# Kernel optimization log

Measured on AMD Instinct MI355X. Metric: run time of the kernel, lower is better.

## Reference

```python
import jax, jax.numpy as jnp
import numpy as np

# dims
T, B, N, H = 16, 8, 8, 128            # time, batch, num_schemas, schema_dim
C, IH, IW = 32, 16, 16                # conv_dims
TASK, ACT, REW = 128, 16, 1
HEADS = 7
TAR = TASK + ACT + REW                # 145
CTX = H + TAR                         # 273 context_dim
CONV_FLAT = C * IH * IW               # 8192
MEM_IN = CONV_FLAT + H + CTX          # 8593


def setup_inputs() -> dict:
    key = jax.random.key(0)
    ks = jax.random.split(key, 20)
    def n(k, shape, s=0.02):
        return jax.random.normal(k, shape, dtype=jnp.float32) * s
    D = HEADS * H
    return {
        "image": jax.random.normal(ks[0], (T, B, C, IH, IW), dtype=jnp.float32),
        "task_action_reward": jax.random.normal(ks[1], (T, B, TAR), dtype=jnp.float32),
        # MultiHeadedAttention params
        "Wq_w": n(ks[2], (D, CTX)), "Wq_b": jnp.zeros((D,), jnp.float32),
        "Wk_w": n(ks[3], (D, H)),   "Wk_b": jnp.zeros((D,), jnp.float32),
        "Wv_w": n(ks[4], (D, H)),   "Wv_b": jnp.zeros((D,), jnp.float32),
        "Wo_w": n(ks[5], (H, D)),   "Wo_b": jnp.zeros((H,), jnp.float32),
        # TopdownFeatureAttention: N per-query linears (stacked) + 1x1 conv
        "td_w": n(ks[6], (N, C, CTX)), "td_b": jnp.zeros((N, C), jnp.float32),
        "conv_w": n(ks[7], (C, C)), "conv_b": jnp.zeros((C,), jnp.float32),
        # ListStructuredRnn: N per-schema LSTM cells (PyTorch gate order i,f,g,o)
        "Wih": n(ks[8], (N, 4 * H, MEM_IN)), "Whh": n(ks[9], (N, 4 * H, H)),
        "bih": jnp.zeros((N, 4 * H), jnp.float32), "bhh": jnp.zeros((N, 4 * H), jnp.float32),
    }


def reference(image, task_action_reward, Wq_w, Wq_b, Wk_w, Wk_b, Wv_w, Wv_b,
              Wo_w, Wo_b, td_w, td_b, conv_w, conv_b, Wih, Whh, bih, bhh):
    f32 = image.dtype
    # prev_state=None path: prev_h is zeros for all timesteps
    prev_h = jnp.zeros((T, B, N, H), f32)
    # schema_context = duplicate task_action_reward over schemas, cat prev_h -> (T,B,N,CTX)
    ctx = jnp.concatenate(
        [jnp.broadcast_to(task_action_reward[:, :, None, :], (T, B, N, TAR)), prev_h], axis=-1)
    # keys = cat(prev_h, zeros) along schema axis -> (T,B,N+1,H)
    keys = jnp.concatenate([prev_h, jnp.zeros((T, B, 1, H), f32)], axis=2)

    # --- MultiHeadedAttention (no mask; dropout unused in forward) ---
    q = (ctx @ Wq_w.T + Wq_b).reshape(T, B, N, HEADS, H)
    k = (keys @ Wk_w.T + Wk_b).reshape(T, B, N + 1, HEADS, H)
    v = (keys @ Wv_w.T + Wv_b).reshape(T, B, N + 1, HEADS, H)
    scores = jnp.einsum('tbqhd,tbkhd->tbhqk', q, k) / jnp.sqrt(jnp.asarray(H, f32))
    attn = jax.nn.softmax(scores, axis=-1)
    xatt = jnp.einsum('tbhqk,tbkhd->tbqhd', attn, v).reshape(T, B, N, HEADS * H)
    shared = xatt @ Wo_w.T + Wo_b                      # (T,B,N,H)

    # --- TopdownFeatureAttention: per-query linear -> sigmoid channel gate -> 1x1 conv ---
    gate = jax.nn.sigmoid(jnp.einsum('tbnx,ncx->tbnc', ctx, td_w) + td_b)   # (T,B,N,C)
    modulated = image[:, :, None] * gate[..., None, None]                    # (T,B,N,C,IH,IW)
    conv = jnp.einsum('tbnchw,dc->tbndhw', modulated, conv_w) + conv_b[:, None, None]
    schema_updates = conv.reshape(T, B, N, CONV_FLAT)

    # --- per-schema LSTMs over time (zero initial state) ---
    mem = jnp.concatenate([schema_updates, shared, ctx], axis=-1)            # (T,B,N,MEM_IN)
    xg = jnp.einsum('tbni,ngi->tbng', mem, Wih) + bih + bhh                  # (T,B,N,4H)

    def step(carry, g_t):
        h, c = carry
        g = g_t + jnp.einsum('bnh,ngh->bng', h, Whh)
        i, f, gg, o = jnp.split(g, 4, axis=-1)
        c = jax.nn.sigmoid(f) * c + jax.nn.sigmoid(i) * jnp.tanh(gg)
        h = jax.nn.sigmoid(o) * jnp.tanh(c)
        return (h, c), h

    z = jnp.zeros((B, N, H), f32)
    (hT, cT), hs = jax.lax.scan(step, (z, z), xg)
    outs = hs.reshape(T, B, N * H)
    return outs, hT, cT
```

## Files before the change

kernel.cpp:

```cpp
#include <hip/hip_runtime.h>

#define T_   16
#define B_   8
#define N_   8
#define H_   128
#define C_   32
#define HW_  256
#define TAR_ 145
#define G4H  512
#define MEMIN 8593
#define AK   8512
#define XGN  524288
#define KSTEP 64
#define PANEL_E 136192

typedef __attribute__((ext_vector_type(8))) short short8v;
typedef __attribute__((ext_vector_type(4))) float f32x4;
typedef __attribute__((ext_vector_type(4), aligned(4))) float f32x4u;

__device__ __forceinline__ float bf2f(unsigned short u){
  return __uint_as_float(((unsigned int)u) << 16);
}
__device__ __forceinline__ unsigned short f2bf(float x){
  unsigned int b = __float_as_uint(x);
  return (unsigned short)((b + 0x7fffu + ((b >> 16) & 1u)) >> 16);
}
__device__ __forceinline__ unsigned pkbf(float lo, float hi){
  return __builtin_amdgcn_perm(__float_as_uint(hi) + 0x8000u,
                               __float_as_uint(lo) + 0x8000u, 0x07060302u);
}
__device__ __forceinline__ float bflo(unsigned w){ return __uint_as_float(w << 16); }
__device__ __forceinline__ float bfhi(unsigned w){ return __uint_as_float(w & 0xffff0000u); }
__device__ __forceinline__ float sigf(float x){ return 1.f/(1.f + expf(-x)); }

__device__ __forceinline__ void gl_lds16(const void* g, void* l){
  __builtin_amdgcn_global_load_lds(
      (const __attribute__((address_space(1))) unsigned int*)g,
      (__attribute__((address_space(3))) unsigned int*)l, 16, 0, 0);
}
__device__ __forceinline__ void gl_lds4(const void* g, void* l){
  __builtin_amdgcn_global_load_lds(
      (const __attribute__((address_space(1))) unsigned int*)g,
      (__attribute__((address_space(3))) unsigned int*)l, 4, 0, 0);
}

__global__ void k_shared(const float* __restrict__ WvB, const float* __restrict__ WoW,
                         const float* __restrict__ WoB, float* __restrict__ sh){
  const int h = blockIdx.x, lane = threadIdx.x;
  float acc = 0.f;
  for(int d = lane; d < 896; d += 64) acc += WvB[d] * WoW[h*896 + d];
  for(int s = 32; s; s >>= 1) acc += __shfl_down(acc, s);
  if(lane == 0) sh[h] = acc + WoB[h];
}

__global__ __launch_bounds__(256) void k_gate(const float* __restrict__ tar,
                                              const float* __restrict__ tdw,
                                              const float* __restrict__ tdb,
                                              float* __restrict__ gate){
  __shared__ float twS[32*145];
  __shared__ float taS[16*145];
  const int tb0 = blockIdx.x * 16, n = blockIdx.y, tid = threadIdx.x;
  for(int i = tid; i < 32*145; i += 256){
    int c = i / 145, x = i - c*145;
    twS[i] = tdw[(n*32 + c)*273 + x];
  }
  for(int i = tid; i < 16*145; i += 256)
    taS[i] = tar[tb0*145 + i];
  __syncthreads();
  for(int o = tid; o < 512; o += 256){
    int r = o >> 5, c = o & 31;
    float a = tdb[n*32 + c];
    const float* tr = &taS[r*145];
    const float* tw = &twS[c*145];
    for(int x = 0; x < 145; ++x) a += tr[x]*tw[x];
    gate[((tb0 + r)*N_ + n)*C_ + c] = 1.f/(1.f + expf(-a));
  }
}

__global__ __launch_bounds__(256) void k_conv2(
    const float* __restrict__ img, const float* __restrict__ gate,
    const float* __restrict__ cw, const float* __restrict__ cb,
    const float* __restrict__ sh, const float* __restrict__ tar,
    unsigned short* __restrict__ mem)
{
  __shared__ float imgS[8192];
  __shared__ float cwgT[1024];
  const int tb = blockIdx.x, n = blockIdx.y;
  const int hw = threadIdx.x;
  for(int i = hw; i < 8192; i += 256)
    imgS[i] = img[(size_t)tb*8192 + i];
  for(int i = hw; i < 1024; i += 256){
    const int c = i >> 5, d = i & 31;
    cwgT[i] = cw[d*32 + c] * gate[(tb*8 + n)*32 + c];
  }
  __syncthreads();
  f32x4 acc[8];
  #pragma unroll
  for(int dq = 0; dq < 8; ++dq){
    const f32x4u cv = *(const f32x4u*)&cb[dq*4];
    acc[dq].x = cv.x; acc[dq].y = cv.y; acc[dq].z = cv.z; acc[dq].w = cv.w;
  }
  #pragma unroll 4
  for(int c = 0; c < 32; ++c){
    const float iv = imgS[c*256 + hw];
    #pragma unroll
    for(int dq = 0; dq < 8; ++dq){
      const f32x4 w = *(const f32x4*)&cwgT[c*32 + dq*4];
      acc[dq].x += iv*w.x; acc[dq].y += iv*w.y;
      acc[dq].z += iv*w.z; acc[dq].w += iv*w.w;
    }
  }
  unsigned short* mrow = mem + (size_t)(n*128 + tb)*AK;
  #pragma unroll
  for(int dq = 0; dq < 8; ++dq){
    mrow[(dq*4 + 0)*256 + hw] = f2bf(acc[dq].x);
    mrow[(dq*4 + 1)*256 + hw] = f2bf(acc[dq].y);
    mrow[(dq*4 + 2)*256 + hw] = f2bf(acc[dq].z);
    mrow[(dq*4 + 3)*256 + hw] = f2bf(acc[dq].w);
  }
  for(int i = hw; i < 320; i += 256){
    if(i < 128)      mrow[8192 + i]       = f2bf(sh[i]);
    else if(i < 273) mrow[8320 + i - 128] = f2bf(tar[tb*TAR_ + i - 128]);
    else             mrow[8465 + i - 273] = 0;
  }
}

__global__ __launch_bounds__(256) void k_wprep(
    const float* __restrict__ Wih, unsigned short* __restrict__ wsB)
{
  const unsigned J = 4358144u;
  const unsigned stride = gridDim.x * 256u;
  for(unsigned j = blockIdx.x*256u + threadIdx.x; j < J; j += stride){
    const unsigned r  = j / 1064u;
    const unsigned k0 = (j - r*1064u) * 8u;
    const float* src = Wih + (size_t)r*MEMIN + k0;
    const f32x4u v0 = *(const f32x4u*)src;
    const f32x4u v1 = *(const f32x4u*)(src + 4);
    uint4 o;
    o.x = pkbf(v0.x, v0.y); o.y = pkbf(v0.z, v0.w);
    o.z = pkbf(v1.x, v1.y); o.w = pkbf(v1.z, v1.w);
    const unsigned n = r >> 9, g512 = r & 511u;
    const unsigned gt = g512 >> 4, g = g512 & 15u;
    const unsigned kb = k0 >> 6, kin = k0 & 63u;
    const unsigned ksw = (((kin >> 3) ^ (g & 7u)) << 3);
    unsigned short* dst = wsB + (size_t)(n*32u + gt)*PANEL_E
                          + kb*1024u + g*64u + ksw;
    *(uint4*)dst = o;
  }
}

__global__ __launch_bounds__(256) void k_gemm6(
    const unsigned short* __restrict__ mem, const unsigned short* __restrict__ wsB,
    float* __restrict__ xg4)
{
  __shared__ unsigned short Abuf[2][128*64];
  __shared__ unsigned short Bbuf[2][16*64];
  const int gt = blockIdx.x, n = blockIdx.y, ks = blockIdx.z;
  const int tid = threadIdx.x;
  const int wv = tid >> 6, ln = tid & 63;
  const int lr = ln & 15, lg = ln >> 4;
  const int g0 = gt*16;
  const int kbeg = (ks == 0) ? 0 : 2176 + (ks - 1)*2112;
  const int nsteps = (ks == 0) ? 34 : 33;
  const unsigned short* An = mem + (size_t)n*128*AK;
  const char* panelB = (const char*)(wsB + (size_t)(n*32 + gt)*PANEL_E);

#define STAGE6(bb, kk) do{                                                     \
    _Pragma("unroll")                                                          \
    for(int i_ = 0; i_ < 4; ++i_){                                             \
      const int ci_ = i_*256 + tid;                                            \
      const int row_ = ci_ >> 3;                                               \
      const unsigned short* src_ = An + (size_t)row_*AK + (kk)                 \
                                   + (((ci_ & 7) ^ (row_ & 7)) << 3);          \
      gl_lds16(src_, &Abuf[bb][(i_*256 + wv*64)*8]);                           \
    }                                                                          \
    _Pragma("unroll")                                                          \
    for(int j_ = 0; j_ < 2; ++j_){                                             \
      const char* srcB_ = panelB + (size_t)((kk) >> 6)*2048                    \
                          + wv*512 + j_*256 + ln*4;                            \
      gl_lds4(srcB_, (char*)&Bbuf[bb][0] + wv*512 + j_*256);                   \
    }                                                                          \
  }while(0)

  f32x4 acc0 = {0.f,0.f,0.f,0.f};
  f32x4 acc1 = {0.f,0.f,0.f,0.f};

  STAGE6(0, kbeg);
  __syncthreads();

  int b = 0;
  for(int t = 0; t < nsteps; ++t){
    if(t + 1 < nsteps) STAGE6(b^1, kbeg + (t+1)*KSTEP);
    #pragma unroll
    for(int s = 0; s < 2; ++s){
      const int jb = (s*4 + lg) ^ (lr & 7);
      const short8v bf = *(const short8v*)&Bbuf[b][lr*64 + jb*8];
      const short8v a0 = *(const short8v*)&Abuf[b][(wv*32 + lr)*64 + jb*8];
      const short8v a1 = *(const short8v*)&Abuf[b][(wv*32 + 16 + lr)*64 + jb*8];
      acc0 = __builtin_amdgcn_mfma_f32_16x16x32_bf16(a0, bf, acc0, 0, 0, 0);
      acc1 = __builtin_amdgcn_mfma_f32_16x16x32_bf16(a1, bf, acc1, 0, 0, 0);
    }
    __syncthreads();
    b ^= 1;
  }
#undef STAGE6

  float* dst = xg4 + (size_t)ks*XGN;
  const int c0 = g0 + lr;
  const int r0 = wv*32 + lg*4, r1 = r0 + 16;
  #pragma unroll
  for(int j = 0; j < 4; ++j){
    dst[(size_t)((r0 + j)*8 + n)*G4H + c0] = acc0[j];
    dst[(size_t)((r1 + j)*8 + n)*G4H + c0] = acc1[j];
  }
}

__global__ __launch_bounds__(256) void k_gemm5(
    const unsigned short* __restrict__ mem, const float* __restrict__ Wih,
    float* __restrict__ xg4)
{
  __shared__ unsigned short Abuf[2][128*64];
  __shared__ float          Bbuf[2][16*64];
  const int gt = blockIdx.x, n = blockIdx.y, ks = blockIdx.z;
  const int tid = threadIdx.x;
  const int wv = tid >> 6, ln = tid & 63;
  const int lr = ln & 15, lg = ln >> 4;
  const int g0 = gt*16;
  const int kbeg = (ks == 0) ? 0 : 2176 + (ks - 1)*2112;
  const int nsteps = (ks == 0) ? 34 : 33;
  const unsigned short* An = mem + (size_t)n*128*AK;
  const float* Bn = Wih + (size_t)(n*G4H + g0)*MEMIN;

#define STAGE5(bb, kk) do{                                                     \
    _Pragma("unroll")                                                          \
    for(int i_ = 0; i_ < 4; ++i_){                                             \
      const int ci_ = i_*256 + tid;                                            \
      const int row_ = ci_ >> 3;                                               \
      const unsigned short* src_ = An + (size_t)row_*AK + (kk)                 \
                                   + (((ci_ & 7) ^ (row_ & 7)) << 3);          \
      gl_lds16(src_, &Abuf[bb][(i_*256 + wv*64)*8]);                           \
    }                                                                          \
    _Pragma("unroll")                                                          \
    for(int q_ = 0; q_ < 4; ++q_){                                             \
      const int idx_ = q_*256 + tid;                                           \
      const int g_ = idx_ >> 6;                                                \
      const int kd_ = idx_ & 63;                                               \
      const float* srcB_ = Bn + (size_t)g_*MEMIN + (kk)                        \
                           + ((((kd_ >> 3) ^ (g_ & 7)) << 3) + (kd_ & 7));     \
      gl_lds4(srcB_, &Bbuf[bb][q_*256 + wv*64]);                               \
    }                                                                          \
  }while(0)

  f32x4 acc0 = {0.f,0.f,0.f,0.f};
  f32x4 acc1 = {0.f,0.f,0.f,0.f};

  STAGE5(0, kbeg);
  if(nsteps > 1) STAGE5(1, kbeg + KSTEP);

  int b = 0;
  for(int t = 0; t < nsteps; ++t){
    if(t < nsteps - 1){
      asm volatile("s_waitcnt vmcnt(8)" ::: "memory");
    } else {
      asm volatile("s_waitcnt vmcnt(0)" ::: "memory");
    }
    __builtin_amdgcn_s_barrier();
    #pragma unroll
    for(int s = 0; s < 2; ++s){
      const int jb = (s*4 + lg) ^ (lr & 7);
      const float* bp = &Bbuf[b][lr*64 + jb*8];
      const f32x4 blo = *(const f32x4*)bp;
      const f32x4 bhi = *(const f32x4*)(bp + 4);
      short8v bf;
      unsigned* u = (unsigned*)&bf;
      u[0] = pkbf(blo.x, blo.y); u[1] = pkbf(blo.z, blo.w);
      u[2] = pkbf(bhi.x, bhi.y); u[3] = pkbf(bhi.z, bhi.w);
      const short8v a0 = *(const short8v*)&Abuf[b][(wv*32 + lr)*64 + jb*8];
      const short8v a1 = *(const short8v*)&Abuf[b][(wv*32 + 16 + lr)*64 + jb*8];
      acc0 = __builtin_amdgcn_mfma_f32_16x16x32_bf16(a0, bf, acc0, 0, 0, 0);
      acc1 = __builtin_amdgcn_mfma_f32_16x16x32_bf16(a1, bf, acc1, 0, 0, 0);
    }
    __builtin_amdgcn_s_barrier();
    if(t + 2 < nsteps) STAGE5(b, kbeg + (t+2)*KSTEP);
    b ^= 1;
  }
#undef STAGE5

  float* dst = xg4 + (size_t)ks*XGN;
  const int c0 = g0 + lr;
  const int r0 = wv*32 + lg*4, r1 = r0 + 16;
  #pragma unroll
  for(int j = 0; j < 4; ++j){
    dst[(size_t)((r0 + j)*8 + n)*G4H + c0] = acc0[j];
    dst[(size_t)((r1 + j)*8 + n)*G4H + c0] = acc1[j];
  }
}

__global__ __launch_bounds__(512) void k_lstm2(
    const float* __restrict__ xg4, const float* __restrict__ Whh,
    const float* __restrict__ bih, const float* __restrict__ bhh,
    float* __restrict__ out)
{
  __shared__ float hS[128];
  __shared__ float preS[512];
  const int bn = blockIdx.x;
  const int n = bn & 7, b = bn >> 3;
  const int g = threadIdx.x;

  unsigned wr[64];
  const float* wrow = Whh + (size_t)(n*G4H + g)*H_;
  #pragma unroll
  for(int i = 0; i < 32; ++i){
    const f32x4 w = *(const f32x4*)(wrow + i*4);
    wr[2*i]   = pkbf(w.x, w.y);
    wr[2*i+1] = pkbf(w.z, w.w);
  }
  const float bias = bih[n*G4H + g] + bhh[n*G4H + g];
  if(g < 128) hS[g] = 0.f;
  float cc = 0.f;
  __syncthreads();

  for(int t = 0; t < 16; ++t){
    const size_t xb = (size_t)((t*8 + b)*8 + n)*G4H + g;
    float acc = bias + xg4[xb] + xg4[xb + XGN] + xg4[xb + 2*XGN] + xg4[xb + 3*XGN];
    #pragma unroll
    for(int q = 0; q < 32; ++q){
      const f32x4 hv = *(const f32x4*)&hS[q*4];
      const unsigned w0 = wr[2*q], w1 = wr[2*q+1];
      acc += hv.x*bflo(w0) + hv.y*bfhi(w0) + hv.z*bflo(w1) + hv.w*bfhi(w1);
    }
    preS[g] = acc;
    __syncthreads();
    if(g < 128){
      const float iv = sigf(preS[g]);
      const float fv = sigf(preS[128 + g]);
      const float gv = tanhf(preS[256 + g]);
      const float ov = sigf(preS[384 + g]);
      cc = fv*cc + iv*gv;
      const float hn = ov*tanhf(cc);
      hS[g] = hn;
      out[(t*8 + b)*1024 + n*128 + g] = hn;
      if(t == 15){
        out[131072 + (b*8 + n)*128 + g] = hn;
        out[139264 + (b*8 + n)*128 + g] = cc;
      }
    }
    __syncthreads();
  }
}

extern "C" void kernel_launch(void* const* d_in, const int* in_sizes, int n_in,
                              void* d_out, int out_size, void* d_ws, size_t ws_size,
                              hipStream_t stream)
{
  (void)in_sizes; (void)n_in; (void)out_size;
  const float* img  = (const float*)d_in[0];
  const float* tar  = (const float*)d_in[1];
  const float* WvB  = (const float*)d_in[7];
  const float* WoW  = (const float*)d_in[8];
  const float* WoB  = (const float*)d_in[9];
  const float* tdw  = (const float*)d_in[10];
  const float* tdb  = (const float*)d_in[11];
  const float* cw   = (const float*)d_in[12];
  const float* cb   = (const float*)d_in[13];
  const float* Wih  = (const float*)d_in[14];
  const float* Whh  = (const float*)d_in[15];
  const float* bih  = (const float*)d_in[16];
  const float* bhh  = (const float*)d_in[17];

  float* wsf   = (float*)d_ws;
  float* gatew = wsf;
  float* shw   = wsf + 32768;
  float* xg4w  = wsf + 32896;
  unsigned short* memA = (unsigned short*)((char*)d_ws + 8520192);
  unsigned short* wsB  = (unsigned short*)((char*)d_ws + 25952768);
  const size_t WS_A  = 25952768;
  const size_t WS_AP = 25952768 + (size_t)256*PANEL_E*2;

  k_shared<<<128, 64, 0, stream>>>(WvB, WoW, WoB, shw);
  k_gate<<<dim3(8, 8), 256, 0, stream>>>(tar, tdw, tdb, gatew);
  k_conv2<<<dim3(128, 8), 256, 0, stream>>>(img, gatew, cw, cb, shw, tar, memA);

  if(ws_size >= WS_AP){
    k_wprep<<<2048, 256, 0, stream>>>(Wih, wsB);
    k_gemm6<<<dim3(32, 8, 4), 256, 0, stream>>>(memA, wsB, xg4w);
  } else if(ws_size >= WS_A){
    k_gemm5<<<dim3(32, 8, 4), 256, 0, stream>>>(memA, Wih, xg4w);
  }
  k_lstm2<<<64, 512, 0, stream>>>(xg4w, Whh, bih, bhh, (float*)d_out);
}
```

Before: 146.9 us.

## Replace weight-prep plus split-K GEMM with single fp32-B 4-stage pipelined GEMM

Removes the separate bf16 weight-packing kernel and the 4-way split-K of the input-projection GEMM. A new kernel streams fp32 Wih straight into LDS through a 4-slot ring buffer with explicit vmcnt waits, converts it to bf16 at fragment load, and runs the full K range in one block per (schema, gate tile), 256 blocks. The LSTM kernel now takes the number of partial sums as a parameter, so it reads one partial instead of four. The cost is twice the B bytes staged in LDS, more dynamic shared memory per block, and less parallelism than the 1024-block split-K grid.

```diff
diff --git a/kernel.cpp b/kernel.cpp
--- a/kernel.cpp
+++ b/kernel.cpp
@@ -12,7 +12,6 @@
 #define AK   8512
 #define XGN  524288
 #define KSTEP 64
-#define PANEL_E 136192
 
 typedef __attribute__((ext_vector_type(8))) short short8v;
 typedef __attribute__((ext_vector_type(4))) float f32x4;
@@ -125,93 +124,138 @@
   }
 }
 
-__global__ __launch_bounds__(256) void k_wprep(
-    const float* __restrict__ Wih, unsigned short* __restrict__ wsB)
-{
-  const unsigned J = 4358144u;
-  const unsigned stride = gridDim.x * 256u;
-  for(unsigned j = blockIdx.x*256u + threadIdx.x; j < J; j += stride){
-    const unsigned r  = j / 1064u;
-    const unsigned k0 = (j - r*1064u) * 8u;
-    const float* src = Wih + (size_t)r*MEMIN + k0;
-    const f32x4u v0 = *(const f32x4u*)src;
-    const f32x4u v1 = *(const f32x4u*)(src + 4);
-    uint4 o;
-    o.x = pkbf(v0.x, v0.y); o.y = pkbf(v0.z, v0.w);
-    o.z = pkbf(v1.x, v1.y); o.w = pkbf(v1.z, v1.w);
-    const unsigned n = r >> 9, g512 = r & 511u;
-    const unsigned gt = g512 >> 4, g = g512 & 15u;
-    const unsigned kb = k0 >> 6, kin = k0 & 63u;
-    const unsigned ksw = (((kin >> 3) ^ (g & 7u)) << 3);
-    unsigned short* dst = wsB + (size_t)(n*32u + gt)*PANEL_E
-                          + kb*1024u + g*64u + ksw;
-    *(uint4*)dst = o;
-  }
-}
-
-__global__ __launch_bounds__(256) void k_gemm6(
-    const unsigned short* __restrict__ mem, const unsigned short* __restrict__ wsB,
-    float* __restrict__ xg4)
-{
-  __shared__ unsigned short Abuf[2][128*64];
-  __shared__ unsigned short Bbuf[2][16*64];
-  const int gt = blockIdx.x, n = blockIdx.y, ks = blockIdx.z;
+__global__ __launch_bounds__(256) void k_gemm7(
+    const unsigned short* __restrict__ mem, const float* __restrict__ Wih,
+    float* __restrict__ xg)
+{
+  extern __shared__ char smem7[];
+  unsigned short (*Abuf)[128*64] = (unsigned short(*)[128*64])smem7;
+  float (*Bbuf)[16*64] = (float(*)[16*64])(smem7 + 4*128*64*2);
+  const int bid = blockIdx.x;
+  const int n = bid & 7, gt = bid >> 3;
   const int tid = threadIdx.x;
   const int wv = tid >> 6, ln = tid & 63;
   const int lr = ln & 15, lg = ln >> 4;
   const int g0 = gt*16;
-  const int kbeg = (ks == 0) ? 0 : 2176 + (ks - 1)*2112;
-  const int nsteps = (ks == 0) ? 34 : 33;
   const unsigned short* An = mem + (size_t)n*128*AK;
-  const char* panelB = (const char*)(wsB + (size_t)(n*32 + gt)*PANEL_E);
-
-#define STAGE6(bb, kk) do{                                                     \
+  const float* Bn = Wih + (size_t)(n*G4H + g0)*MEMIN;
+
+#define STAGE7(sl, kk) do{                                                     \
     _Pragma("unroll")                                                          \
     for(int i_ = 0; i_ < 4; ++i_){                                             \
       const int ci_ = i_*256 + tid;                                            \
       const int row_ = ci_ >> 3;                                               \
       const unsigned short* src_ = An + (size_t)row_*AK + (kk)                 \
                                    + (((ci_ & 7) ^ (row_ & 7)) << 3);          \
-      gl_lds16(src_, &Abuf[bb][(i_*256 + wv*64)*8]);                           \
+      gl_lds16(src_, &Abuf[sl][(i_*256 + wv*64)*8]);                           \
     }                                                                          \
     _Pragma("unroll")                                                          \
-    for(int j_ = 0; j_ < 2; ++j_){                                             \
-      const char* srcB_ = panelB + (size_t)((kk) >> 6)*2048                    \
-                          + wv*512 + j_*256 + ln*4;                            \
-      gl_lds4(srcB_, (char*)&Bbuf[bb][0] + wv*512 + j_*256);                   \
+    for(int q_ = 0; q_ < 4; ++q_){                                             \
+      const int idx_ = q_*256 + tid;                                           \
+      const int g_ = idx_ >> 6;                                                \
+      const int kd_ = idx_ & 63;                                               \
+      const float* srcB_ = Bn + (size_t)g_*MEMIN + (kk)                        \
+                           + ((((kd_ >> 3) ^ (g_ & 7)) << 3) + (kd_ & 7));     \
+      gl_lds4(srcB_, &Bbuf[sl][q_*256 + wv*64]);                               \
     }                                                                          \
   }while(0)
 
   f32x4 acc0 = {0.f,0.f,0.f,0.f};
   f32x4 acc1 = {0.f,0.f,0.f,0.f};
 
-  STAGE6(0, kbeg);
-  __syncthreads();
-
-  int b = 0;
-  for(int t = 0; t < nsteps; ++t){
-    if(t + 1 < nsteps) STAGE6(b^1, kbeg + (t+1)*KSTEP);
+  STAGE7(0, 0);
+  STAGE7(1, KSTEP);
+  STAGE7(2, 2*KSTEP);
+
+  for(int t = 0; t < 133; ++t){
+    if(t < 131){
+      asm volatile("s_waitcnt vmcnt(16)" ::: "memory");
+    } else if(t == 131){
+      asm volatile("s_waitcnt vmcnt(8)" ::: "memory");
+    } else {
+      asm volatile("s_waitcnt vmcnt(0)" ::: "memory");
+    }
+    __builtin_amdgcn_s_barrier();
+    const int sl = t & 3;
     #pragma unroll
     for(int s = 0; s < 2; ++s){
       const int jb = (s*4 + lg) ^ (lr & 7);
-      const short8v bf = *(const short8v*)&Bbuf[b][lr*64 + jb*8];
-      const short8v a0 = *(const short8v*)&Abuf[b][(wv*32 + lr)*64 + jb*8];
-      const short8v a1 = *(const short8v*)&Abuf[b][(wv*32 + 16 + lr)*64 + jb*8];
+      const float* bp = &Bbuf[sl][lr*64 + jb*8];
+      const f32x4 blo = *(const f32x4*)bp;
+      const f32x4 bhi = *(const f32x4*)(bp + 4);
+      short8v bf;
+      unsigned* u = (unsigned*)&bf;
+      u[0] = pkbf(blo.x, blo.y); u[1] = pkbf(blo.z, blo.w);
+      u[2] = pkbf(bhi.x, bhi.y); u[3] = pkbf(bhi.z, bhi.w);
+      const short8v a0 = *(const short8v*)&Abuf[sl][(wv*32 + lr)*64 + jb*8];
+      const short8v a1 = *(const short8v*)&Abuf[sl][(wv*32 + 16 + lr)*64 + jb*8];
       acc0 = __builtin_amdgcn_mfma_f32_16x16x32_bf16(a0, bf, acc0, 0, 0, 0);
       acc1 = __builtin_amdgcn_mfma_f32_16x16x32_bf16(a1, bf, acc1, 0, 0, 0);
     }
-    __syncthreads();
-    b ^= 1;
-  }
-#undef STAGE6
-
-  float* dst = xg4 + (size_t)ks*XGN;
+    if(t + 3 < 133) STAGE7((t + 3) & 3, (t + 3)*KSTEP);
+  }
+#undef STAGE7
+
   const int c0 = g0 + lr;
   const int r0 = wv*32 + lg*4, r1 = r0 + 16;
   #pragma unroll
   for(int j = 0; j < 4; ++j){
-    dst[(size_t)((r0 + j)*8 + n)*G4H + c0] = acc0[j];
-    dst[(size_t)((r1 + j)*8 + n)*G4H + c0] = acc1[j];
+    xg[(size_t)((r0 + j)*8 + n)*G4H + c0] = acc0[j];
+    xg[(size_t)((r1 + j)*8 + n)*G4H + c0] = acc1[j];
+  }
+}
+
+__global__ __launch_bounds__(512) void k_lstm2(
+    const float* __restrict__ xg4, int nsum, const float* __restrict__ Whh,
+    const float* __restrict__ bih, const float* __restrict__ bhh,
+    float* __restrict__ out)
+{
+  __shared__ float hS[128];
+  __shared__ float preS[512];
+  const int bn = blockIdx.x;
+  const int n = bn & 7, b = bn >> 3;
+  const int g = threadIdx.x;
+
+  unsigned wr[64];
+  const float* wrow = Whh + (size_t)(n*G4H + g)*H_;
+  #pragma unroll
+  for(int i = 0; i < 32; ++i){
+    const f32x4 w = *(const f32x4*)(wrow + i*4);
+    wr[2*i]   = pkbf(w.x, w.y);
+    wr[2*i+1] = pkbf(w.z, w.w);
+  }
+  const float bias = bih[n*G4H + g] + bhh[n*G4H + g];
+  if(g < 128) hS[g] = 0.f;
+  float cc = 0.f;
+  __syncthreads();
+
+  for(int t = 0; t < 16; ++t){
+    const size_t xb = (size_t)((t*8 + b)*8 + n)*G4H + g;
+    float acc = bias;
+    for(int u = 0; u < nsum; ++u) acc += xg4[xb + (size_t)u*XGN];
+    #pragma unroll
+    for(int q = 0; q < 32; ++q){
+      const f32x4 hv = *(const f32x4*)&hS[q*4];
+      const unsigned w0 = wr[2*q], w1 = wr[2*q+1];
+      acc += hv.x*bflo(w0) + hv.y*bfhi(w0) + hv.z*bflo(w1) + hv.w*bfhi(w1);
+    }
+    preS[g] = acc;
+    __syncthreads();
+    if(g < 128){
+      const float iv = sigf(preS[g]);
+      const float fv = sigf(preS[128 + g]);
+      const float gv = tanhf(preS[256 + g]);
+      const float ov = sigf(preS[384 + g]);
+      cc = fv*cc + iv*gv;
+      const float hn = ov*tanhf(cc);
+      hS[g] = hn;
+      out[(t*8 + b)*1024 + n*128 + g] = hn;
+      if(t == 15){
+        out[131072 + (b*8 + n)*128 + g] = hn;
+        out[139264 + (b*8 + n)*128 + g] = cc;
+      }
+    }
+    __syncthreads();
   }
 }
 
@@ -296,59 +340,6 @@
   }
 }
 
-__global__ __launch_bounds__(512) void k_lstm2(
-    const float* __restrict__ xg4, const float* __restrict__ Whh,
-    const float* __restrict__ bih, const float* __restrict__ bhh,
-    float* __restrict__ out)
-{
-  __shared__ float hS[128];
-  __shared__ float preS[512];
-  const int bn = blockIdx.x;
-  const int n = bn & 7, b = bn >> 3;
-  const int g = threadIdx.x;
-
-  unsigned wr[64];
-  const float* wrow = Whh + (size_t)(n*G4H + g)*H_;
-  #pragma unroll
-  for(int i = 0; i < 32; ++i){
-    const f32x4 w = *(const f32x4*)(wrow + i*4);
-    wr[2*i]   = pkbf(w.x, w.y);
-    wr[2*i+1] = pkbf(w.z, w.w);
-  }
-  const float bias = bih[n*G4H + g] + bhh[n*G4H + g];
-  if(g < 128) hS[g] = 0.f;
-  float cc = 0.f;
-  __syncthreads();
-
-  for(int t = 0; t < 16; ++t){
-    const size_t xb = (size_t)((t*8 + b)*8 + n)*G4H + g;
-    float acc = bias + xg4[xb] + xg4[xb + XGN] + xg4[xb + 2*XGN] + xg4[xb + 3*XGN];
-    #pragma unroll
-    for(int q = 0; q < 32; ++q){
-      const f32x4 hv = *(const f32x4*)&hS[q*4];
-      const unsigned w0 = wr[2*q], w1 = wr[2*q+1];
-      acc += hv.x*bflo(w0) + hv.y*bfhi(w0) + hv.z*bflo(w1) + hv.w*bfhi(w1);
-    }
-    preS[g] = acc;
-    __syncthreads();
-    if(g < 128){
-      const float iv = sigf(preS[g]);
-      const float fv = sigf(preS[128 + g]);
-      const float gv = tanhf(preS[256 + g]);
-      const float ov = sigf(preS[384 + g]);
-      cc = fv*cc + iv*gv;
-      const float hn = ov*tanhf(cc);
-      hS[g] = hn;
-      out[(t*8 + b)*1024 + n*128 + g] = hn;
-      if(t == 15){
-        out[131072 + (b*8 + n)*128 + g] = hn;
-        out[139264 + (b*8 + n)*128 + g] = cc;
-      }
-    }
-    __syncthreads();
-  }
-}
-
 extern "C" void kernel_launch(void* const* d_in, const int* in_sizes, int n_in,
                               void* d_out, int out_size, void* d_ws, size_t ws_size,
                               hipStream_t stream)
@@ -371,21 +362,21 @@
   float* wsf   = (float*)d_ws;
   float* gatew = wsf;
   float* shw   = wsf + 32768;
-  float* xg4w  = wsf + 32896;
+  float* xgw   = wsf + 32896;
   unsigned short* memA = (unsigned short*)((char*)d_ws + 8520192);
-  unsigned short* wsB  = (unsigned short*)((char*)d_ws + 25952768);
-  const size_t WS_A  = 25952768;
-  const size_t WS_AP = 25952768 + (size_t)256*PANEL_E*2;
+  const size_t WS_7 = 8520192 + (size_t)8*128*AK*2;
 
   k_shared<<<128, 64, 0, stream>>>(WvB, WoW, WoB, shw);
   k_gate<<<dim3(8, 8), 256, 0, stream>>>(tar, tdw, tdb, gatew);
   k_conv2<<<dim3(128, 8), 256, 0, stream>>>(img, gatew, cw, cb, shw, tar, memA);
 
-  if(ws_size >= WS_AP){
-    k_wprep<<<2048, 256, 0, stream>>>(Wih, wsB);
-    k_gemm6<<<dim3(32, 8, 4), 256, 0, stream>>>(memA, wsB, xg4w);
-  } else if(ws_size >= WS_A){
-    k_gemm5<<<dim3(32, 8, 4), 256, 0, stream>>>(memA, Wih, xg4w);
-  }
-  k_lstm2<<<64, 512, 0, stream>>>(xg4w, Whh, bih, bhh, (float*)d_out);
-}
+  if(ws_size >= WS_7){
+    (void)hipFuncSetAttribute((const void*)k_gemm7,
+                              hipFuncAttributeMaxDynamicSharedMemorySize, 81920);
+    k_gemm7<<<256, 256, 81920, stream>>>(memA, Wih, xgw);
+    k_lstm2<<<64, 512, 0, stream>>>(xgw, 1, Whh, bih, bhh, (float*)d_out);
+  } else {
+    k_gemm5<<<dim3(32, 8, 4), 256, 0, stream>>>(memA, Wih, xgw);
+    k_lstm2<<<64, 512, 0, stream>>>(xgw, 4, Whh, bih, bhh, (float*)d_out);
+  }
+}
```

New measurement: 125.1 us. 1.17x faster.

## Fuse Wih bf16 conversion into GEMM via LDS-resident weight panel

Applied to the files above, without the earlier changes.

Drops the separate k_wprep kernel that converted Wih to a swizzled bf16 panel in workspace. Each GEMM block now loads its 16-row fp32 weight slice once, converts it to bf16 and keeps the whole K-slice in about 68KB of dynamic LDS. It then streams only A through a two-deep prefetch that waits on vmcnt instead of using full syncthreads. This removes one launch and a write-then-reread of the converted weights. The cost is heavy LDS use per block, which limits occupancy, plus a serial conversion prologue before the MFMA loop.

```diff
diff --git a/kernel.cpp b/kernel.cpp
--- a/kernel.cpp
+++ b/kernel.cpp
@@ -12,7 +12,6 @@
 #define AK   8512
 #define XGN  524288
 #define KSTEP 64
-#define PANEL_E 136192
 
 typedef __attribute__((ext_vector_type(8))) short short8v;
 typedef __attribute__((ext_vector_type(4))) float f32x4;
@@ -125,85 +124,80 @@
   }
 }
 
-__global__ __launch_bounds__(256) void k_wprep(
-    const float* __restrict__ Wih, unsigned short* __restrict__ wsB)
-{
-  const unsigned J = 4358144u;
-  const unsigned stride = gridDim.x * 256u;
-  for(unsigned j = blockIdx.x*256u + threadIdx.x; j < J; j += stride){
-    const unsigned r  = j / 1064u;
-    const unsigned k0 = (j - r*1064u) * 8u;
-    const float* src = Wih + (size_t)r*MEMIN + k0;
-    const f32x4u v0 = *(const f32x4u*)src;
-    const f32x4u v1 = *(const f32x4u*)(src + 4);
-    uint4 o;
-    o.x = pkbf(v0.x, v0.y); o.y = pkbf(v0.z, v0.w);
-    o.z = pkbf(v1.x, v1.y); o.w = pkbf(v1.z, v1.w);
-    const unsigned n = r >> 9, g512 = r & 511u;
-    const unsigned gt = g512 >> 4, g = g512 & 15u;
-    const unsigned kb = k0 >> 6, kin = k0 & 63u;
-    const unsigned ksw = (((kin >> 3) ^ (g & 7u)) << 3);
-    unsigned short* dst = wsB + (size_t)(n*32u + gt)*PANEL_E
-                          + kb*1024u + g*64u + ksw;
-    *(uint4*)dst = o;
-  }
-}
-
-__global__ __launch_bounds__(256) void k_gemm6(
-    const unsigned short* __restrict__ mem, const unsigned short* __restrict__ wsB,
+__global__ __launch_bounds__(256) void k_gemm9(
+    const unsigned short* __restrict__ mem, const float* __restrict__ Wih,
     float* __restrict__ xg4)
 {
-  __shared__ unsigned short Abuf[2][128*64];
-  __shared__ unsigned short Bbuf[2][16*64];
-  const int gt = blockIdx.x, n = blockIdx.y, ks = blockIdx.z;
+  extern __shared__ char smem9[];
+  unsigned short* Blds = (unsigned short*)smem9;
+  unsigned short (*Abuf)[8192] = (unsigned short(*)[8192])(smem9 + 69632);
+  const int n = blockIdx.x, gt = blockIdx.y, ks = blockIdx.z;
   const int tid = threadIdx.x;
   const int wv = tid >> 6, ln = tid & 63;
   const int lr = ln & 15, lg = ln >> 4;
   const int g0 = gt*16;
   const int kbeg = (ks == 0) ? 0 : 2176 + (ks - 1)*2112;
   const int nsteps = (ks == 0) ? 34 : 33;
+  const int nc = nsteps*8;
   const unsigned short* An = mem + (size_t)n*128*AK;
-  const char* panelB = (const char*)(wsB + (size_t)(n*32 + gt)*PANEL_E);
-
-#define STAGE6(bb, kk) do{                                                     \
+  const float* Bn = Wih + (size_t)(n*G4H + g0)*MEMIN + kbeg;
+
+  const int tot = 16*nc;
+  #pragma unroll 4
+  for(int j0 = 0; j0 < tot; j0 += 256){
+    const int j = j0 + tid;
+    if(j < tot){
+      const int r = j / nc, c = j - r*nc;
+      const float* src = Bn + (size_t)r*MEMIN + c*8;
+      const f32x4u v0 = *(const f32x4u*)src;
+      const f32x4u v1 = *(const f32x4u*)(src + 4);
+      uint4 o;
+      o.x = pkbf(v0.x, v0.y); o.y = pkbf(v0.z, v0.w);
+      o.z = pkbf(v1.x, v1.y); o.w = pkbf(v1.z, v1.w);
+      const int csw = (c & ~7) | ((c & 7) ^ (r & 7));
+      *(uint4*)((char*)Blds + r*4352 + csw*16) = o;
+    }
+  }
+  __syncthreads();
+
+#define STAGEA(bb, kk) do{                                                     \
     _Pragma("unroll")                                                          \
     for(int i_ = 0; i_ < 4; ++i_){                                             \
       const int ci_ = i_*256 + tid;                                            \
       const int row_ = ci_ >> 3;                                               \
-      const unsigned short* src_ = An + (size_t)row_*AK + (kk)                 \
-                                   + (((ci_ & 7) ^ (row_ & 7)) << 3);          \
-      gl_lds16(src_, &Abuf[bb][(i_*256 + wv*64)*8]);                           \
-    }                                                                          \
-    _Pragma("unroll")                                                          \
-    for(int j_ = 0; j_ < 2; ++j_){                                             \
-      const char* srcB_ = panelB + (size_t)((kk) >> 6)*2048                    \
-                          + wv*512 + j_*256 + ln*4;                            \
-      gl_lds4(srcB_, (char*)&Bbuf[bb][0] + wv*512 + j_*256);                   \
+      gl_lds16(An + (size_t)row_*AK + (kk) + (((ci_ & 7) ^ (row_ & 7)) << 3),  \
+               (char*)&Abuf[bb][0] + (i_*256 + wv*64)*16);                     \
     }                                                                          \
   }while(0)
 
   f32x4 acc0 = {0.f,0.f,0.f,0.f};
   f32x4 acc1 = {0.f,0.f,0.f,0.f};
 
-  STAGE6(0, kbeg);
-  __syncthreads();
+  STAGEA(0, kbeg);
+  if(nsteps > 1) STAGEA(1, kbeg + KSTEP);
 
   int b = 0;
   for(int t = 0; t < nsteps; ++t){
-    if(t + 1 < nsteps) STAGE6(b^1, kbeg + (t+1)*KSTEP);
+    if(t < nsteps - 1){
+      asm volatile("s_waitcnt vmcnt(4)" ::: "memory");
+    } else {
+      asm volatile("s_waitcnt vmcnt(0)" ::: "memory");
+    }
+    __builtin_amdgcn_s_barrier();
     #pragma unroll
     for(int s = 0; s < 2; ++s){
       const int jb = (s*4 + lg) ^ (lr & 7);
-      const short8v bf = *(const short8v*)&Bbuf[b][lr*64 + jb*8];
+      const short8v bf = *(const short8v*)((char*)Blds + lr*4352 + (t*8 + jb)*16);
       const short8v a0 = *(const short8v*)&Abuf[b][(wv*32 + lr)*64 + jb*8];
       const short8v a1 = *(const short8v*)&Abuf[b][(wv*32 + 16 + lr)*64 + jb*8];
       acc0 = __builtin_amdgcn_mfma_f32_16x16x32_bf16(a0, bf, acc0, 0, 0, 0);
       acc1 = __builtin_amdgcn_mfma_f32_16x16x32_bf16(a1, bf, acc1, 0, 0, 0);
     }
-    __syncthreads();
+    __builtin_amdgcn_s_barrier();
+    if(t + 2 < nsteps) STAGEA(b, kbeg + (t + 2)*KSTEP);
     b ^= 1;
   }
-#undef STAGE6
+#undef STAGEA
 
   float* dst = xg4 + (size_t)ks*XGN;
   const int c0 = g0 + lr;
@@ -212,6 +206,60 @@
   for(int j = 0; j < 4; ++j){
     dst[(size_t)((r0 + j)*8 + n)*G4H + c0] = acc0[j];
     dst[(size_t)((r1 + j)*8 + n)*G4H + c0] = acc1[j];
+  }
+}
+
+__global__ __launch_bounds__(512) void k_lstm2(
+    const float* __restrict__ xg4, int nsum, const float* __restrict__ Whh,
+    const float* __restrict__ bih, const float* __restrict__ bhh,
+    float* __restrict__ out)
+{
+  __shared__ float hS[128];
+  __shared__ float preS[512];
+  const int bn = blockIdx.x;
+  const int n = bn & 7, b = bn >> 3;
+  const int g = threadIdx.x;
+
+  unsigned wr[64];
+  const float* wrow = Whh + (size_t)(n*G4H + g)*H_;
+  #pragma unroll
+  for(int i = 0; i < 32; ++i){
+    const f32x4 w = *(const f32x4*)(wrow + i*4);
+    wr[2*i]   = pkbf(w.x, w.y);
+    wr[2*i+1] = pkbf(w.z, w.w);
+  }
+  const float bias = bih[n*G4H + g] + bhh[n*G4H + g];
+  if(g < 128) hS[g] = 0.f;
+  float cc = 0.f;
+  __syncthreads();
+
+  for(int t = 0; t < 16; ++t){
+    const size_t xb = (size_t)((t*8 + b)*8 + n)*G4H + g;
+    float acc = bias;
+    for(int u = 0; u < nsum; ++u) acc += xg4[xb + (size_t)u*XGN];
+    #pragma unroll
+    for(int q = 0; q < 32; ++q){
+      const f32x4 hv = *(const f32x4*)&hS[q*4];
+      const unsigned w0 = wr[2*q], w1 = wr[2*q+1];
+      acc += hv.x*bflo(w0) + hv.y*bfhi(w0) + hv.z*bflo(w1) + hv.w*bfhi(w1);
+    }
+    preS[g] = acc;
+    __syncthreads();
+    if(g < 128){
+      const float iv = sigf(preS[g]);
+      const float fv = sigf(preS[128 + g]);
+      const float gv = tanhf(preS[256 + g]);
+      const float ov = sigf(preS[384 + g]);
+      cc = fv*cc + iv*gv;
+      const float hn = ov*tanhf(cc);
+      hS[g] = hn;
+      out[(t*8 + b)*1024 + n*128 + g] = hn;
+      if(t == 15){
+        out[131072 + (b*8 + n)*128 + g] = hn;
+        out[139264 + (b*8 + n)*128 + g] = cc;
+      }
+    }
+    __syncthreads();
   }
 }
 
@@ -296,59 +344,6 @@
   }
 }
 
-__global__ __launch_bounds__(512) void k_lstm2(
-    const float* __restrict__ xg4, const float* __restrict__ Whh,
-    const float* __restrict__ bih, const float* __restrict__ bhh,
-    float* __restrict__ out)
-{
-  __shared__ float hS[128];
-  __shared__ float preS[512];
-  const int bn = blockIdx.x;
-  const int n = bn & 7, b = bn >> 3;
-  const int g = threadIdx.x;
-
-  unsigned wr[64];
-  const float* wrow = Whh + (size_t)(n*G4H + g)*H_;
-  #pragma unroll
-  for(int i = 0; i < 32; ++i){
-    const f32x4 w = *(const f32x4*)(wrow + i*4);
-    wr[2*i]   = pkbf(w.x, w.y);
-    wr[2*i+1] = pkbf(w.z, w.w);
-  }
-  const float bias = bih[n*G4H + g] + bhh[n*G4H + g];
-  if(g < 128) hS[g] = 0.f;
-  float cc = 0.f;
-  __syncthreads();
-
-  for(int t = 0; t < 16; ++t){
-    const size_t xb = (size_t)((t*8 + b)*8 + n)*G4H + g;
-    float acc = bias + xg4[xb] + xg4[xb + XGN] + xg4[xb + 2*XGN] + xg4[xb + 3*XGN];
-    #pragma unroll
-    for(int q = 0; q < 32; ++q){
-      const f32x4 hv = *(const f32x4*)&hS[q*4];
-      const unsigned w0 = wr[2*q], w1 = wr[2*q+1];
-      acc += hv.x*bflo(w0) + hv.y*bfhi(w0) + hv.z*bflo(w1) + hv.w*bfhi(w1);
-    }
-    preS[g] = acc;
-    __syncthreads();
-    if(g < 128){
-      const float iv = sigf(preS[g]);
-      const float fv = sigf(preS[128 + g]);
-      const float gv = tanhf(preS[256 + g]);
-      const float ov = sigf(preS[384 + g]);
-      cc = fv*cc + iv*gv;
-      const float hn = ov*tanhf(cc);
-      hS[g] = hn;
-      out[(t*8 + b)*1024 + n*128 + g] = hn;
-      if(t == 15){
-        out[131072 + (b*8 + n)*128 + g] = hn;
-        out[139264 + (b*8 + n)*128 + g] = cc;
-      }
-    }
-    __syncthreads();
-  }
-}
-
 extern "C" void kernel_launch(void* const* d_in, const int* in_sizes, int n_in,
                               void* d_out, int out_size, void* d_ws, size_t ws_size,
                               hipStream_t stream)
@@ -371,21 +366,21 @@
   float* wsf   = (float*)d_ws;
   float* gatew = wsf;
   float* shw   = wsf + 32768;
-  float* xg4w  = wsf + 32896;
+  float* xgw   = wsf + 32896;
   unsigned short* memA = (unsigned short*)((char*)d_ws + 8520192);
-  unsigned short* wsB  = (unsigned short*)((char*)d_ws + 25952768);
-  const size_t WS_A  = 25952768;
-  const size_t WS_AP = 25952768 + (size_t)256*PANEL_E*2;
+  const size_t WS_7 = 8520192 + (size_t)8*128*AK*2;
 
   k_shared<<<128, 64, 0, stream>>>(WvB, WoW, WoB, shw);
   k_gate<<<dim3(8, 8), 256, 0, stream>>>(tar, tdw, tdb, gatew);
   k_conv2<<<dim3(128, 8), 256, 0, stream>>>(img, gatew, cw, cb, shw, tar, memA);
 
-  if(ws_size >= WS_AP){
-    k_wprep<<<2048, 256, 0, stream>>>(Wih, wsB);
-    k_gemm6<<<dim3(32, 8, 4), 256, 0, stream>>>(memA, wsB, xg4w);
-  } else if(ws_size >= WS_A){
-    k_gemm5<<<dim3(32, 8, 4), 256, 0, stream>>>(memA, Wih, xg4w);
-  }
-  k_lstm2<<<64, 512, 0, stream>>>(xg4w, Whh, bih, bhh, (float*)d_out);
-}
+  if(ws_size >= WS_7){
+    (void)hipFuncSetAttribute((const void*)k_gemm9,
+                              hipFuncAttributeMaxDynamicSharedMemorySize, 102400);
+    k_gemm9<<<dim3(8, 32, 4), 256, 102400, stream>>>(memA, Wih, xgw);
+    k_lstm2<<<64, 512, 0, stream>>>(xgw, 4, Whh, bih, bhh, (float*)d_out);
+  } else {
+    k_gemm5<<<dim3(32, 8, 4), 256, 0, stream>>>(memA, Wih, xgw);
+    k_lstm2<<<64, 512, 0, stream>>>(xgw, 4, Whh, bih, bhh, (float*)d_out);
+  }
+}
```

Result: no change. 149.9 us (+2.0%).
